# Performance work log

Hardware: AMD Instinct MI355X
Metric: run time of the kernel (lower is better)

Reference implementation:

```python
import jax, jax.numpy as jnp
import numpy as np

N = 100000      # nodes
E = 1600000     # edges (before self-loops)
IN = 128        # in_channels
HID = 16        # hidden per head
HEADS = 8
OUT = 16        # out_channels (classes)
NEG_SLOPE = 0.2


def setup_inputs() -> dict:
    key = jax.random.key(0)
    ks = jax.random.split(key, 10)
    x = jax.random.normal(ks[0], (N, IN), jnp.float32)
    edge_index = jax.random.randint(ks[1], (2, E), 0, N, jnp.int32)
    g = lambda k, shape, fan: (jax.random.normal(k, shape, jnp.float32)
                               * (1.0 / np.sqrt(fan)).astype(np.float32))
    # layer 1: in -> heads*hid
    W1 = g(ks[2], (IN, HEADS * HID), IN)
    att_src1 = g(ks[3], (HEADS, HID), HID)
    att_dst1 = g(ks[4], (HEADS, HID), HID)
    b1 = jnp.zeros((HEADS * HID,), jnp.float32)
    # layer 2: heads*hid -> out, 1 head, concat=False
    W2 = g(ks[5], (HEADS * HID, OUT), HEADS * HID)
    att_src2 = g(ks[6], (1, OUT), OUT)
    att_dst2 = g(ks[7], (1, OUT), OUT)
    b2 = jnp.zeros((OUT,), jnp.float32)
    return dict(x=x, edge_index=edge_index, W1=W1, att_src1=att_src1,
                att_dst1=att_dst1, b1=b1, W2=W2, att_src2=att_src2,
                att_dst2=att_dst2, b2=b2)


def gat_conv(x, src, dst, W, a_src, a_dst, b, concat):
    """PyG-style GATConv (eval mode). src->dst message flow."""
    num_nodes = x.shape[0]
    H, C = a_src.shape
    h = (x @ W).reshape(num_nodes, H, C)                      # [N,H,C]
    # per-node attention halves, gathered to edges
    e = (h * a_src).sum(-1)[src] + (h * a_dst).sum(-1)[dst]   # [Etot,H]
    e = jax.nn.leaky_relu(e, NEG_SLOPE)
    # segment softmax over edges grouped by destination node
    emax = jax.ops.segment_max(e, dst, num_segments=num_nodes)    # [N,H]
    ee = jnp.exp(e - emax[dst])
    denom = jax.ops.segment_sum(ee, dst, num_segments=num_nodes)  # [N,H]
    alpha = ee / (denom[dst] + 1e-16)                              # [Etot,H]
    # weighted scatter-aggregate of source features
    msg = h[src] * alpha[:, :, None]                               # [Etot,H,C]
    out = jax.ops.segment_sum(msg, dst, num_segments=num_nodes)    # [N,H,C]
    out = out.reshape(num_nodes, H * C) if concat else out.mean(axis=1)
    return out + b


def reference(x, edge_index, W1, att_src1, att_dst1, b1,
              W2, att_src2, att_dst2, b2):
    # add self loops (PyG GATConv default)
    loop = jnp.arange(N, dtype=edge_index.dtype)
    src = jnp.concatenate([edge_index[0], loop])
    dst = jnp.concatenate([edge_index[1], loop])

    h = gat_conv(x, src, dst, W1, att_src1, att_dst1, b1, concat=True)
    embeddings = jax.nn.elu(h)
    logits = gat_conv(embeddings, src, dst, W2, att_src2, att_dst2, b2,
                      concat=False)
    return jax.nn.log_softmax(logits, axis=1), embeddings
```

## Files before the change

kernel.cpp:

```cpp
#include <hip/hip_runtime.h>
#include <hip/hip_bf16.h>
#include <math.h>

#define N_NODES 100000
#define E_EDGES 1600000
#define ETOT    (E_EDGES + N_NODES)
#define NEG     0.2f

#define SH        8
#define NBUCK     ((N_NODES + 255) >> 8)
#define BIN_TILE  2048
#define NBIN      ((E_EDGES + BIN_TILE - 1) / BIN_TILE)
#define CAP_B     5120

#define NMFMA     ((N_NODES + 63) / 64)
#define G_A       782
#define G_B       (NMFMA - G_A)

typedef __attribute__((ext_vector_type(8))) short bf16x8;
typedef __attribute__((ext_vector_type(4))) float f32x4;
typedef __attribute__((ext_vector_type(2))) short bf16p;

__device__ inline float lrelu(float x) { return x > 0.f ? x : NEG * x; }
__device__ inline float bflo(unsigned int b) { return __uint_as_float(b << 16); }
__device__ inline float bfhi(unsigned int b) { return __uint_as_float(b & 0xFFFF0000u); }
__device__ inline unsigned short f2bf(float f) {
    unsigned int u = __float_as_uint(f);
    return (unsigned short)((u + 0x7FFFu + ((u >> 16) & 1u)) >> 16);
}

__device__ inline float dot2bf(unsigned int wp, unsigned int hp, float c) {
#if __has_builtin(__builtin_amdgcn_fdot2_f32_bf16)
    return __builtin_amdgcn_fdot2_f32_bf16(__builtin_bit_cast(bf16p, wp),
                                           __builtin_bit_cast(bf16p, hp),
                                           c, false);
#else
    return fmaf(bflo(wp), bflo(hp), fmaf(bfhi(wp), bfhi(hp), c));
#endif
}

__global__ __launch_bounds__(256) void k_wt(const float* __restrict__ W,
                                            unsigned short* __restrict__ wtg) {
    int t = blockIdx.x * 256 + threadIdx.x;
    if (t >= 128 * 128) return;
    int n = t >> 7, k = t & 127;
    wtg[t] = f2bf(W[k * 128 + n]);
}

__device__ __forceinline__ void gemm1_role(
    int n0, int t, unsigned short (*xb)[136],
    const float* __restrict__ x, const unsigned short* __restrict__ wtg,
    const float* __restrict__ asrc, const float* __restrict__ adst,
    __hip_bfloat16* __restrict__ h1b, float* __restrict__ s1,
    float* __restrict__ d1) {
#pragma unroll
    for (int i = 0; i < 8; ++i) {
        int i4 = t + i * 256;
        int r = i4 >> 5;
        int c = (i4 & 31) * 4;
        float4 v = make_float4(0.f, 0.f, 0.f, 0.f);
        if (n0 + r < N_NODES) v = *(const float4*)(x + (size_t)(n0 + r) * 128 + c);
        xb[r][c + 0] = f2bf(v.x);
        xb[r][c + 1] = f2bf(v.y);
        xb[r][c + 2] = f2bf(v.z);
        xb[r][c + 3] = f2bf(v.w);
    }
    __syncthreads();

    int l = t & 63, wv = t >> 6;
    int col = l & 15, q4 = l >> 4;
    int rbase = wv * 16;
    int koff = q4 * 8;

    bf16x8 a[4];
#pragma unroll
    for (int st = 0; st < 4; ++st)
        a[st] = *(const bf16x8*)&xb[rbase + col][st * 32 + koff];

    int nodeb = n0 + rbase + q4 * 4;
#pragma unroll
    for (int nt = 0; nt < 8; ++nt) {
        f32x4 acc = {0.f, 0.f, 0.f, 0.f};
        const unsigned short* wrow = wtg + (size_t)(nt * 16 + col) * 128 + koff;
#pragma unroll
        for (int st = 0; st < 4; ++st) {
            bf16x8 b = *(const bf16x8*)(wrow + st * 32);
            acc = __builtin_amdgcn_mfma_f32_16x16x32_bf16(a[st], b, acc, 0, 0, 0);
        }
        float as_v = asrc[nt * 16 + col];
        float ad_v = adst[nt * 16 + col];
#pragma unroll
        for (int r = 0; r < 4; ++r) {
            int node = nodeb + r;
            if (node < N_NODES)
                h1b[(size_t)node * 128 + nt * 16 + col] = __float2bfloat16(acc[r]);
            float ps = acc[r] * as_v, pd = acc[r] * ad_v;
#pragma unroll
            for (int ofs = 1; ofs < 16; ofs <<= 1) {
                ps += __shfl_xor(ps, ofs, 64);
                pd += __shfl_xor(pd, ofs, 64);
            }
            if (col == 0 && node < N_NODES) {
                s1[node * 8 + nt] = ps;
                d1[node * 8 + nt] = pd;
            }
        }
    }
}

union SmemBin {
    struct {
        int2 st[BIN_TILE];
        int  hist[NBUCK + 1];
        int  lstart[NBUCK];
        int  gbase[NBUCK];
        int  tsum[256];
    } b;
    unsigned short xb[64][136];
};

__global__ __launch_bounds__(256) void k_parBin(
    const int* __restrict__ src, const int* __restrict__ dst,
    int* __restrict__ gcur, int2* __restrict__ coo,
    const float* __restrict__ x, const unsigned short* __restrict__ wtg,
    const float* __restrict__ asrc, const float* __restrict__ adst,
    __hip_bfloat16* __restrict__ h1b, float* __restrict__ s1,
    float* __restrict__ d1) {
    __shared__ SmemBin sm;
    int bid = blockIdx.x, t = threadIdx.x;
    if (bid & 1) {
        gemm1_role((bid >> 1) * 64, t, sm.xb, x, wtg, asrc, adst, h1b, s1, d1);
        return;
    }
    int wb = bid >> 1;
    int e0 = wb * BIN_TILE;
    int nE = min(BIN_TILE, E_EDGES - e0);
    for (int i = t; i <= NBUCK; i += 256) sm.b.hist[i] = 0;
    __syncthreads();
    for (int i = t; i < nE; i += 256)
        atomicAdd(&sm.b.hist[dst[e0 + i] >> SH], 1);
    __syncthreads();
    int i0 = 2 * t, i1 = 2 * t + 1;
    int h0 = (i0 < NBUCK) ? sm.b.hist[i0] : 0;
    int h1v = (i1 < NBUCK) ? sm.b.hist[i1] : 0;
    int s = h0 + h1v;
    sm.b.tsum[t] = s;
    __syncthreads();
    for (int ofs = 1; ofs < 256; ofs <<= 1) {
        int u = (t >= ofs) ? sm.b.tsum[t - ofs] : 0;
        __syncthreads();
        sm.b.tsum[t] += u;
        __syncthreads();
    }
    int pre = sm.b.tsum[t] - s;
    if (i0 < NBUCK) sm.b.hist[i0] = pre;
    if (i1 < NBUCK) sm.b.hist[i1] = pre + h0;
    if (t == 255) sm.b.hist[NBUCK] = sm.b.tsum[255];
    __syncthreads();
    for (int i = t; i < NBUCK; i += 256) {
        int st_ = sm.b.hist[i];
        int cnt = sm.b.hist[i + 1] - st_;
        sm.b.lstart[i] = st_;
        if (cnt > 0) sm.b.gbase[i] = i * CAP_B + atomicAdd(&gcur[i], cnt);
    }
    __syncthreads();
    for (int i = t; i < nE; i += 256) {
        int sv = src[e0 + i], dv = dst[e0 + i];
        int p = atomicAdd(&sm.b.hist[dv >> SH], 1);
        sm.b.st[p] = make_int2(sv, dv);
    }
    __syncthreads();
    for (int i = t; i < nE; i += 256) {
        int2 e = sm.b.st[i];
        int b2 = e.y >> SH;
        int slot = sm.b.gbase[b2] + (i - sm.b.lstart[b2]);
        slot = min(slot, (b2 + 1) * CAP_B - 1);
        coo[slot] = e;
    }
}

__global__ __launch_bounds__(256) void k_scanb(const int* __restrict__ gcur,
                                               int* __restrict__ bbase,
                                               int* __restrict__ off) {
    __shared__ int tsum[256];
    int t = threadIdx.x;
    int i0 = 2 * t, i1 = 2 * t + 1;
    int a = 0, b = 0;
    if (i0 < NBUCK) a = min(gcur[i0], CAP_B) + min(256, N_NODES - (i0 << SH));
    if (i1 < NBUCK) b = min(gcur[i1], CAP_B) + min(256, N_NODES - (i1 << SH));
    int s = a + b;
    tsum[t] = s;
    __syncthreads();
    for (int ofs = 1; ofs < 256; ofs <<= 1) {
        int u = (t >= ofs) ? tsum[t - ofs] : 0;
        __syncthreads();
        tsum[t] += u;
        __syncthreads();
    }
    int pre = tsum[t] - s;
    if (i0 < NBUCK) bbase[i0] = pre;
    if (i1 < NBUCK) bbase[i1] = pre + a;
    if (t == 0) off[N_NODES] = ETOT;
}

union SmemFine {
    struct {
        int ldeg[256];
        int lpre[256];
        int lsrc[CAP_B + 256];
    } f;
    unsigned short xb[64][136];
};

__global__ __launch_bounds__(256) void k_parFine(
    const int2* __restrict__ coo, const int* __restrict__ gcur,
    const int* __restrict__ bbase, int* __restrict__ off,
    int* __restrict__ csr,
    const float* __restrict__ x, const unsigned short* __restrict__ wtg,
    const float* __restrict__ asrc, const float* __restrict__ adst,
    __hip_bfloat16* __restrict__ h1b, float* __restrict__ s1,
    float* __restrict__ d1) {
    __shared__ SmemFine sm;
    int bid = blockIdx.x, t = threadIdx.x;
    bool isFine = (bid % 3 == 0) && (bid / 3 < NBUCK);
    if (!isFine) {
        int gid = bid - bid / 3 - 1;
        gemm1_role((G_A + gid) * 64, t, sm.xb, x, wtg, asrc, adst, h1b, s1, d1);
        return;
    }
    int b = bid / 3;
    int n0 = b << SH;
    int nn = min(256, N_NODES - n0);
    int ecnt = min(gcur[b], CAP_B);
    int base = bbase[b];
    const int2* seg = coo + (size_t)b * CAP_B;

    sm.f.ldeg[t] = 0;
    __syncthreads();
    for (int i = t; i < ecnt; i += 256)
        atomicAdd(&sm.f.ldeg[seg[i].y - n0], 1);
    __syncthreads();
    int d = (t < nn) ? sm.f.ldeg[t] + 1 : 0;
    sm.f.lpre[t] = d;
    __syncthreads();
    for (int ofs = 1; ofs < 256; ofs <<= 1) {
        int u = (t >= ofs) ? sm.f.lpre[t - ofs] : 0;
        __syncthreads();
        sm.f.lpre[t] += u;
        __syncthreads();
    }
    int myoff = sm.f.lpre[t] - d;
    __syncthreads();
    if (t < nn) {
        off[n0 + t] = base + myoff;
        sm.f.lsrc[myoff] = n0 + t;
        sm.f.ldeg[t] = myoff + 1;
    }
    __syncthreads();
    for (int i = t; i < ecnt; i += 256) {
        int2 e = seg[i];
        int p = atomicAdd(&sm.f.ldeg[e.y - n0], 1);
        sm.f.lsrc[p] = e.x;
    }
    __syncthreads();
    int tot = ecnt + nn;
    for (int i = t; i < tot; i += 256)
        csr[base + i] = sm.f.lsrc[i];
}

__global__ __launch_bounds__(256) void k_l1(
    const int* __restrict__ off, const int* __restrict__ csr,
    const float* __restrict__ s1, const float* __restrict__ d1,
    const uint4* __restrict__ h1q, const float* __restrict__ b1,
    float* __restrict__ emb) {
    int t = threadIdx.x;
    int node = blockIdx.x * 4 + (t >> 6);
    int l = t & 63;
    int g = l >> 4, q = l & 15;
    int hb = q >> 1;
    int lo = off[node], hi = off[node + 1];
    float dvh = d1[node * 8 + hb];

    float acc[8];
#pragma unroll
    for (int c = 0; c < 8; ++c) acc[c] = 0.f;
    float den = 0.f;

    int idx = lo + g;
    bool have = (idx + 4 < hi);
    int sa = 0, sb = 0;
    uint4 ba = make_uint4(0, 0, 0, 0), bb = make_uint4(0, 0, 0, 0);
    float sva = 0.f, svb = 0.f;
    if (have) {
        sa = csr[idx]; sb = csr[idx + 4];
        ba = h1q[(size_t)sa * 16 + q];
        bb = h1q[(size_t)sb * 16 + q];
        sva = s1[sa * 8 + hb];
        svb = s1[sb * 8 + hb];
    }
    while (have) {
        int nidx = idx + 8;
        bool nhave = (nidx + 4 < hi);
        int na = 0, nb = 0;
        uint4 nba = make_uint4(0, 0, 0, 0), nbb = make_uint4(0, 0, 0, 0);
        float nsa = 0.f, nsb = 0.f;
        if (nhave) {
            na = csr[nidx]; nb = csr[nidx + 4];
            nba = h1q[(size_t)na * 16 + q];
            nbb = h1q[(size_t)nb * 16 + q];
            nsa = s1[na * 8 + hb];
            nsb = s1[nb * 8 + hb];
        }
        float w0 = __expf(lrelu(sva + dvh));
        float w1 = __expf(lrelu(svb + dvh));
        den += w0 + w1;
        unsigned int wp;
        asm("v_cvt_pk_bf16_f32 %0, %1, %2" : "=v"(wp) : "v"(w0), "v"(w1));
        unsigned int p0, p1;
        p0 = __builtin_amdgcn_perm(bb.x, ba.x, 0x05040100u);
        p1 = __builtin_amdgcn_perm(bb.x, ba.x, 0x07060302u);
        acc[0] = dot2bf(wp, p0, acc[0]);
        acc[1] = dot2bf(wp, p1, acc[1]);
        p0 = __builtin_amdgcn_perm(bb.y, ba.y, 0x05040100u);
        p1 = __builtin_amdgcn_perm(bb.y, ba.y, 0x07060302u);
        acc[2] = dot2bf(wp, p0, acc[2]);
        acc[3] = dot2bf(wp, p1, acc[3]);
        p0 = __builtin_amdgcn_perm(bb.z, ba.z, 0x05040100u);
        p1 = __builtin_amdgcn_perm(bb.z, ba.z, 0x07060302u);
        acc[4] = dot2bf(wp, p0, acc[4]);
        acc[5] = dot2bf(wp, p1, acc[5]);
        p0 = __builtin_amdgcn_perm(bb.w, ba.w, 0x05040100u);
        p1 = __builtin_amdgcn_perm(bb.w, ba.w, 0x07060302u);
        acc[6] = dot2bf(wp, p0, acc[6]);
        acc[7] = dot2bf(wp, p1, acc[7]);
        sa = na; sb = nb; ba = nba; bb = nbb; sva = nsa; svb = nsb;
        idx = nidx; have = nhave;
    }
    if (idx < hi) {
        int sc = csr[idx];
        uint4 bv = h1q[(size_t)sc * 16 + q];
        float w = __expf(lrelu(s1[sc * 8 + hb] + dvh));
        den += w;
        acc[0] = fmaf(w, bflo(bv.x), acc[0]);
        acc[1] = fmaf(w, bfhi(bv.x), acc[1]);
        acc[2] = fmaf(w, bflo(bv.y), acc[2]);
        acc[3] = fmaf(w, bfhi(bv.y), acc[3]);
        acc[4] = fmaf(w, bflo(bv.z), acc[4]);
        acc[5] = fmaf(w, bfhi(bv.z), acc[5]);
        acc[6] = fmaf(w, bflo(bv.w), acc[6]);
        acc[7] = fmaf(w, bfhi(bv.w), acc[7]);
    }
#pragma unroll
    for (int c = 0; c < 8; ++c) {
        acc[c] += __shfl_xor(acc[c], 16, 64);
        acc[c] += __shfl_xor(acc[c], 32, 64);
    }
    den += __shfl_xor(den, 16, 64);
    den += __shfl_xor(den, 32, 64);

    if (l < 16) {
        float r = 1.f / den;
        float vv[8];
#pragma unroll
        for (int c = 0; c < 8; ++c) {
            float v = acc[c] * r + b1[8 * q + c];
            vv[c] = v > 0.f ? v : expm1f(v);
        }
        float4* ep = (float4*)(emb + (size_t)node * 128);
        ep[2 * q]     = make_float4(vv[0], vv[1], vv[2], vv[3]);
        ep[2 * q + 1] = make_float4(vv[4], vv[5], vv[6], vv[7]);
    }
}

__global__ __launch_bounds__(256) void k_gemm2(
    const float* __restrict__ emb, const float* __restrict__ W,
    const float* __restrict__ asrc, const float* __restrict__ adst,
    __hip_bfloat16* __restrict__ h2b, float* __restrict__ s2,
    float* __restrict__ d2) {
    __shared__ float xs[16][129];
    int n0 = blockIdx.x * 16;
    int t = threadIdx.x;
#pragma unroll
    for (int i = 0; i < 8; ++i) {
        int idx = t + i * 256;
        xs[idx >> 7][idx & 127] = emb[(long)n0 * 128 + idx];
    }
    __syncthreads();
    int j = t & 15, sub = t >> 4;
    float acc = 0.f;
    for (int k = 0; k < 128; ++k) acc = fmaf(xs[sub][k], W[k * 16 + j], acc);
    int n = n0 + sub;
    h2b[(long)n * 16 + j] = __float2bfloat16(acc);
    float ps = acc * asrc[j], pd = acc * adst[j];
#pragma unroll
    for (int off = 8; off; off >>= 1) {
        ps += __shfl_down(ps, off, 16);
        pd += __shfl_down(pd, off, 16);
    }
    if (j == 0) { s2[n] = ps; d2[n] = pd; }
}

__global__ __launch_bounds__(256) void k_l2(
    const int* __restrict__ off, const int* __restrict__ csr,
    const float* __restrict__ s2, const float* __restrict__ d2,
    const unsigned int* __restrict__ h2w, const float* __restrict__ b2,
    float* __restrict__ logits) {
    int t = threadIdx.x;
    int node = blockIdx.x * 4 + (t >> 6);
    int l = t & 63;
    int g = l >> 3, p = l & 7;
    int lo = off[node], hi = off[node + 1];
    float dv = d2[node];

    float ax = 0.f, ay = 0.f, den = 0.f;
    for (int idx = lo + g; idx < hi; idx += 8) {
        int s = csr[idx];
        float w = __expf(lrelu(s2[s] + dv));
        den += w;
        unsigned int bv = h2w[(size_t)s * 8 + p];
        ax = fmaf(w, bflo(bv), ax);
        ay = fmaf(w, bfhi(bv), ay);
    }
#pragma unroll
    for (int ofs = 8; ofs < 64; ofs <<= 1) {
        ax += __shfl_xor(ax, ofs, 64);
        ay += __shfl_xor(ay, ofs, 64);
        den += __shfl_xor(den, ofs, 64);
    }
    float r = 1.f / den;
    float v0 = ax * r + b2[2 * p], v1 = ay * r + b2[2 * p + 1];
    float mm = fmaxf(v0, v1);
#pragma unroll
    for (int ofs = 1; ofs < 8; ofs <<= 1) mm = fmaxf(mm, __shfl_xor(mm, ofs, 8));
    float sm = __expf(v0 - mm) + __expf(v1 - mm);
#pragma unroll
    for (int ofs = 1; ofs < 8; ofs <<= 1) sm += __shfl_xor(sm, ofs, 8);
    if (g == 0) {
        float ls = logf(sm);
        logits[node * 16 + 2 * p]     = v0 - mm - ls;
        logits[node * 16 + 2 * p + 1] = v1 - mm - ls;
    }
}

extern "C" void kernel_launch(void* const* d_in, const int* in_sizes, int n_in,
                              void* d_out, int out_size, void* d_ws, size_t ws_size,
                              hipStream_t stream) {
    const float* x   = (const float*)d_in[0];
    const int*   ei  = (const int*)d_in[1];
    const float* W1  = (const float*)d_in[2];
    const float* as1 = (const float*)d_in[3];
    const float* ad1 = (const float*)d_in[4];
    const float* b1  = (const float*)d_in[5];
    const float* W2  = (const float*)d_in[6];
    const float* as2 = (const float*)d_in[7];
    const float* ad2 = (const float*)d_in[8];
    const float* b2  = (const float*)d_in[9];

    float* out    = (float*)d_out;
    float* logits = out;
    float* emb    = out + (size_t)N_NODES * 16;

    float* ws    = (float*)d_ws;
    unsigned int* h1w = (unsigned int*)ws;
    int2*  coo   = (int2*)(h1w + (size_t)N_NODES * 64);
    float* s1    = (float*)(coo + (size_t)NBUCK * CAP_B);
    float* d1    = s1 + (size_t)N_NODES * 8;
    unsigned int* h2w = (unsigned int*)(d1 + (size_t)N_NODES * 8);
    float* s2    = (float*)(h2w + (size_t)N_NODES * 8);
    float* d2v   = s2 + (size_t)N_NODES;
    int*   offs  = (int*)(d2v + (size_t)N_NODES);
    int*   csr   = offs + N_NODES + 2;
    int*   gcur  = csr + ETOT;
    int*   bbase = gcur + NBUCK;
    unsigned short* wtg = (unsigned short*)(bbase + NBUCK);

    const int* srcp = ei;
    const int* dstp = ei + E_EDGES;

    hipMemsetAsync(gcur, 0, (size_t)NBUCK * sizeof(int), stream);

    k_wt<<<64, 256, 0, stream>>>(W1, wtg);
    k_parBin<<<2 * NBIN, 256, 0, stream>>>(srcp, dstp, gcur, coo,
                                           x, wtg, as1, ad1,
                                           (__hip_bfloat16*)h1w, s1, d1);
    k_scanb<<<1, 256, 0, stream>>>(gcur, bbase, offs);
    k_parFine<<<NBUCK + G_B, 256, 0, stream>>>(coo, gcur, bbase, offs, csr,
                                               x, wtg, as1, ad1,
                                               (__hip_bfloat16*)h1w, s1, d1);

    k_l1<<<N_NODES / 4, 256, 0, stream>>>(offs, csr, s1, d1,
                                          (const uint4*)h1w, b1, emb);

    k_gemm2<<<N_NODES / 16, 256, 0, stream>>>(emb, W2, as2, ad2,
                                              (__hip_bfloat16*)h2w, s2, d2v);
    k_l2<<<N_NODES / 4, 256, 0, stream>>>(offs, csr, s2, d2v, h2w, b2, logits);
}
```

Before: 259.3 us.

## Pack layer-1 source scores to bf16, rebalance binning grid, pipeline layer-2 gather

Adds a small kernel that converts the per-node source attention scores s1 to bf16, so the layer-1 aggregation gathers 2-byte values instead of 4-byte floats. BIN_TILE is doubled and the merged bin/GEMM kernel now interleaves one binning block with two GEMM blocks, which halves the number of binning blocks while keeping all GEMM1 tiles in that kernel. The layer-2 aggregation loop is software-pipelined: it prefetches the next indices and features, processes two edges per step with a packed bf16 dot2, and clamps the prefetched index to the segment end. Costs include an extra kernel launch, lower precision in the attention logits, and larger shared-memory staging per binning block.

```diff
diff --git a/kernel.cpp b/kernel.cpp
--- a/kernel.cpp
+++ b/kernel.cpp
@@ -9,7 +9,7 @@
 
 #define SH        8
 #define NBUCK     ((N_NODES + 255) >> 8)
-#define BIN_TILE  2048
+#define BIN_TILE  4096
 #define NBIN      ((E_EDGES + BIN_TILE - 1) / BIN_TILE)
 #define CAP_B     5120
 
@@ -45,6 +45,18 @@
     if (t >= 128 * 128) return;
     int n = t >> 7, k = t & 127;
     wtg[t] = f2bf(W[k * 128 + n]);
+}
+
+__global__ __launch_bounds__(256) void k_pack(const float* __restrict__ s1,
+                                              unsigned short* __restrict__ s1b) {
+    int n = blockIdx.x * 256 + threadIdx.x;
+    if (n >= N_NODES) return;
+    const float4* p = (const float4*)(s1 + (size_t)n * 8);
+    float4 a = p[0], b = p[1];
+    union { unsigned short u[8]; uint4 v; } o;
+    o.u[0] = f2bf(a.x); o.u[1] = f2bf(a.y); o.u[2] = f2bf(a.z); o.u[3] = f2bf(a.w);
+    o.u[4] = f2bf(b.x); o.u[5] = f2bf(b.y); o.u[6] = f2bf(b.z); o.u[7] = f2bf(b.w);
+    *(uint4*)(s1b + (size_t)n * 8) = o.v;
 }
 
 __device__ __forceinline__ void gemm1_role(
@@ -128,11 +140,13 @@
     float* __restrict__ d1) {
     __shared__ SmemBin sm;
     int bid = blockIdx.x, t = threadIdx.x;
-    if (bid & 1) {
-        gemm1_role((bid >> 1) * 64, t, sm.xb, x, wtg, asrc, adst, h1b, s1, d1);
+    bool isBin = (bid % 3 == 0) && (bid / 3 < NBIN);
+    if (!isBin) {
+        int gid = bid - bid / 3 - 1;
+        gemm1_role(gid * 64, t, sm.xb, x, wtg, asrc, adst, h1b, s1, d1);
         return;
     }
-    int wb = bid >> 1;
+    int wb = bid / 3;
     int e0 = wb * BIN_TILE;
     int nE = min(BIN_TILE, E_EDGES - e0);
     for (int i = t; i <= NBUCK; i += 256) sm.b.hist[i] = 0;
@@ -270,7 +284,7 @@
 
 __global__ __launch_bounds__(256) void k_l1(
     const int* __restrict__ off, const int* __restrict__ csr,
-    const float* __restrict__ s1, const float* __restrict__ d1,
+    const unsigned short* __restrict__ s1b, const float* __restrict__ d1,
     const uint4* __restrict__ h1q, const float* __restrict__ b1,
     float* __restrict__ emb) {
     int t = threadIdx.x;
@@ -295,8 +309,8 @@
         sa = csr[idx]; sb = csr[idx + 4];
         ba = h1q[(size_t)sa * 16 + q];
         bb = h1q[(size_t)sb * 16 + q];
-        sva = s1[sa * 8 + hb];
-        svb = s1[sb * 8 + hb];
+        sva = __uint_as_float((unsigned)s1b[(size_t)sa * 8 + hb] << 16);
+        svb = __uint_as_float((unsigned)s1b[(size_t)sb * 8 + hb] << 16);
     }
     while (have) {
         int nidx = idx + 8;
@@ -308,8 +322,8 @@
             na = csr[nidx]; nb = csr[nidx + 4];
             nba = h1q[(size_t)na * 16 + q];
             nbb = h1q[(size_t)nb * 16 + q];
-            nsa = s1[na * 8 + hb];
-            nsb = s1[nb * 8 + hb];
+            nsa = __uint_as_float((unsigned)s1b[(size_t)na * 8 + hb] << 16);
+            nsb = __uint_as_float((unsigned)s1b[(size_t)nb * 8 + hb] << 16);
         }
         float w0 = __expf(lrelu(sva + dvh));
         float w1 = __expf(lrelu(svb + dvh));
@@ -339,7 +353,8 @@
     if (idx < hi) {
         int sc = csr[idx];
         uint4 bv = h1q[(size_t)sc * 16 + q];
-        float w = __expf(lrelu(s1[sc * 8 + hb] + dvh));
+        float sv = __uint_as_float((unsigned)s1b[(size_t)sc * 8 + hb] << 16);
+        float w = __expf(lrelu(sv + dvh));
         den += w;
         acc[0] = fmaf(w, bflo(bv.x), acc[0]);
         acc[1] = fmaf(w, bfhi(bv.x), acc[1]);
@@ -413,7 +428,37 @@
     float dv = d2[node];
 
     float ax = 0.f, ay = 0.f, den = 0.f;
-    for (int idx = lo + g; idx < hi; idx += 8) {
+    int idx = lo + g;
+    int him = hi - 1;
+    if (idx + 8 < hi) {
+        int s0 = csr[idx], s1i = csr[idx + 8];
+        unsigned int pa = h2w[(size_t)s0 * 8 + p];
+        unsigned int pb = h2w[(size_t)s1i * 8 + p];
+        float wa = s2[s0], wb = s2[s1i];
+        int ia = csr[min(idx + 16, him)];
+        int ib = csr[min(idx + 24, him)];
+        while (true) {
+            unsigned int npa = h2w[(size_t)ia * 8 + p];
+            unsigned int npb = h2w[(size_t)ib * 8 + p];
+            float nwa = s2[ia], nwb = s2[ib];
+            int nia = csr[min(idx + 32, him)];
+            int nib = csr[min(idx + 40, him)];
+            float w0 = __expf(lrelu(wa + dv));
+            float w1 = __expf(lrelu(wb + dv));
+            den += w0 + w1;
+            unsigned int wp;
+            asm("v_cvt_pk_bf16_f32 %0, %1, %2" : "=v"(wp) : "v"(w0), "v"(w1));
+            unsigned int p0 = __builtin_amdgcn_perm(pb, pa, 0x05040100u);
+            unsigned int p1 = __builtin_amdgcn_perm(pb, pa, 0x07060302u);
+            ax = dot2bf(wp, p0, ax);
+            ay = dot2bf(wp, p1, ay);
+            idx += 16;
+            if (idx + 8 >= hi) break;
+            pa = npa; pb = npb; wa = nwa; wb = nwb;
+            ia = nia; ib = nib;
+        }
+    }
+    if (idx < hi) {
         int s = csr[idx];
         float w = __expf(lrelu(s2[s] + dv));
         den += w;
@@ -473,6 +518,7 @@
     int*   gcur  = csr + ETOT;
     int*   bbase = gcur + NBUCK;
     unsigned short* wtg = (unsigned short*)(bbase + NBUCK);
+    unsigned short* s1b = wtg + 128 * 128;
 
     const int* srcp = ei;
     const int* dstp = ei + E_EDGES;
@@ -480,15 +526,16 @@
     hipMemsetAsync(gcur, 0, (size_t)NBUCK * sizeof(int), stream);
 
     k_wt<<<64, 256, 0, stream>>>(W1, wtg);
-    k_parBin<<<2 * NBIN, 256, 0, stream>>>(srcp, dstp, gcur, coo,
-                                           x, wtg, as1, ad1,
-                                           (__hip_bfloat16*)h1w, s1, d1);
+    k_parBin<<<NBIN + G_A, 256, 0, stream>>>(srcp, dstp, gcur, coo,
+                                             x, wtg, as1, ad1,
+                                             (__hip_bfloat16*)h1w, s1, d1);
     k_scanb<<<1, 256, 0, stream>>>(gcur, bbase, offs);
     k_parFine<<<NBUCK + G_B, 256, 0, stream>>>(coo, gcur, bbase, offs, csr,
                                                x, wtg, as1, ad1,
                                                (__hip_bfloat16*)h1w, s1, d1);
-
-    k_l1<<<N_NODES / 4, 256, 0, stream>>>(offs, csr, s1, d1,
+    k_pack<<<(N_NODES + 255) / 256, 256, 0, stream>>>(s1, s1b);
+
+    k_l1<<<N_NODES / 4, 256, 0, stream>>>(offs, csr, s1b, d1,
                                           (const uint4*)h1w, b1, emb);
 
     k_gemm2<<<N_NODES / 16, 256, 0, stream>>>(emb, W2, as2, ad2,
```

New measurement: 257.1 us. Within noise of the previous version (-0.9%).
